# Performance work log

Measured on AMD Instinct MI355X. Metric: run time of the kernel, lower is better.

## Reference

```python
import jax, jax.numpy as jnp
import numpy as np

N = 100000       # nodes
E = 1600000      # edges (avg degree 16)
F_IN = 20        # NUM_FEATURES
H = 128          # hidden_channels
EPS = 1e-5       # GraphNorm eps


def setup_inputs() -> dict:
    key = jax.random.key(0)
    ks = jax.random.split(key, 24)
    s = 0.05
    inp = {
        "x": jax.random.normal(ks[0], (N, F_IN), jnp.float32),
        "edge_index": jax.random.randint(ks[1], (2, E), 0, N, dtype=jnp.int32),
    }
    # SAGEConv params: lin_l (neighbors, with bias), lin_r (root, no bias)
    dims = [(F_IN, H), (H, H), (H, H)]
    k = 2
    for i, (din, dout) in enumerate(dims):
        inp[f"Wl{i}"] = jax.random.normal(ks[k], (dout, din), jnp.float32) * s; k += 1
        inp[f"bl{i}"] = jnp.zeros((dout,), jnp.float32)
        inp[f"Wr{i}"] = jax.random.normal(ks[k], (dout, din), jnp.float32) * s; k += 1
        # GraphNorm: weight, bias, mean_scale (alpha)
        inp[f"gw{i}"] = jnp.ones((dout,), jnp.float32)
        inp[f"gb{i}"] = jnp.zeros((dout,), jnp.float32)
        inp[f"ga{i}"] = jnp.ones((dout,), jnp.float32)
    # MLP head: 128 -> 64 -> 32 -> 1
    inp["hW1"] = jax.random.normal(ks[k], (64, H), jnp.float32) * s; k += 1
    inp["hb1"] = jnp.zeros((64,), jnp.float32)
    inp["hW2"] = jax.random.normal(ks[k], (32, 64), jnp.float32) * s; k += 1
    inp["hb2"] = jnp.zeros((32,), jnp.float32)
    inp["hW3"] = jax.random.normal(ks[k], (1, 32), jnp.float32) * s; k += 1
    inp["hb3"] = jnp.zeros((1,), jnp.float32)
    return inp


def _sage(x, src, dst, Wl, bl, Wr):
    # mean aggregation of source features at destination nodes
    deg = jax.ops.segment_sum(jnp.ones((src.shape[0],), x.dtype), dst, num_segments=N)
    agg = jax.ops.segment_sum(x[src], dst, num_segments=N)
    agg = agg / jnp.maximum(deg, 1.0)[:, None]
    return agg @ Wl.T + bl + x @ Wr.T


def _graphnorm(x, w, b, a):
    # single graph (batch=None): stats over all nodes, per channel
    mean = jnp.mean(x, axis=0)
    c = x - a * mean
    var = jnp.mean(c * c, axis=0)
    return w * c * jax.lax.rsqrt(var + EPS) + b


def reference(x, edge_index,
              Wl0, bl0, Wr0, gw0, gb0, ga0,
              Wl1, bl1, Wr1, gw1, gb1, ga1,
              Wl2, bl2, Wr2, gw2, gb2, ga2,
              hW1, hb1, hW2, hb2, hW3, hb3):
    src, dst = edge_index[0], edge_index[1]
    layers = [(Wl0, bl0, Wr0, gw0, gb0, ga0),
              (Wl1, bl1, Wr1, gw1, gb1, ga1),
              (Wl2, bl2, Wr2, gw2, gb2, ga2)]
    h = x
    for (Wl, bl, Wr, gw, gb, ga) in layers:
        h = _sage(h, src, dst, Wl, bl, Wr)
        h = _graphnorm(h, gw, gb, ga)
        h = jax.nn.gelu(h, approximate=False)  # dropout: eval mode (identity)
    h = jax.nn.gelu(h @ hW1.T + hb1, approximate=False)
    h = jax.nn.gelu(h @ hW2.T + hb2, approximate=False)
    out = jax.nn.sigmoid(h @ hW3.T + hb3)
    return out.squeeze(-1)  # [N]
```

## Files before the change

kernel.cpp:

```cpp
#include <hip/hip_runtime.h>
#include <hip/hip_bf16.h>
#include <math.h>

#define NN 100000
#define EE 1600000
#define FIN 20
#define HH 128
#define NBUK 391
#define FILLB 196
#define MMB 782

typedef __attribute__((ext_vector_type(8))) short bf16x8;
typedef __attribute__((ext_vector_type(4))) float f32x4;

__device__ __forceinline__ unsigned short f2b(float x) {
    unsigned int b = __float_as_uint(x);
    unsigned int r = b + 0x7fffu + ((b >> 16) & 1u);
    return (unsigned short)(r >> 16);
}
__device__ __forceinline__ float lof(unsigned int u) { return __uint_as_float(u << 16); }
__device__ __forceinline__ float hif(unsigned int u) { return __uint_as_float(u & 0xffff0000u); }

__device__ __forceinline__ float gelu_exact(float z) {
    return 0.5f * z * (1.0f + erff(z * 0.70710678118654752f));
}

__global__ __launch_bounds__(256) void kb_cnt(const int* __restrict__ dst,
                                              int* __restrict__ bcnt) {
    __shared__ int c[NBUK];
    int t = threadIdx.x;
    for (int i = t; i < NBUK; i += 256) c[i] = 0;
    __syncthreads();
    int e0 = blockIdx.x * 8192;
    #pragma unroll 4
    for (int i = 0; i < 32; ++i) {
        int e = e0 + i * 256 + t;
        if (e < EE) atomicAdd(&c[dst[e] >> 8], 1);
    }
    __syncthreads();
    for (int i = t; i < NBUK; i += 256) if (c[i]) atomicAdd(&bcnt[i], c[i]);
}

__global__ void kb_scan(const int* __restrict__ bcnt, int* __restrict__ bbase,
                        int* __restrict__ cursor) {
    __shared__ int sh[512];
    int t = threadIdx.x;
    int v = (t < NBUK) ? bcnt[t] : 0;
    sh[t] = v;
    __syncthreads();
    for (int off = 1; off < 512; off <<= 1) {
        int add = (t >= off) ? sh[t - off] : 0;
        __syncthreads();
        sh[t] += add;
        __syncthreads();
    }
    if (t < NBUK) {
        int ex = sh[t] - v;
        bbase[t] = ex;
        cursor[t] = ex;
    }
    if (t == NBUK - 1) bbase[NBUK] = sh[t];
}

__global__ __launch_bounds__(256) void kb_fill(const int* __restrict__ src,
        const int* __restrict__ dst, int* __restrict__ cursor,
        unsigned int* __restrict__ pairs) {
    __shared__ int cnt[NBUK], base[NBUK], boff[NBUK];
    int t = threadIdx.x;
    for (int i = t; i < NBUK; i += 256) { cnt[i] = 0; boff[i] = 0; }
    __syncthreads();
    int e0 = blockIdx.x * 8192;
    #pragma unroll 4
    for (int i = 0; i < 32; ++i) {
        int e = e0 + i * 256 + t;
        if (e < EE) atomicAdd(&cnt[dst[e] >> 8], 1);
    }
    __syncthreads();
    for (int i = t; i < NBUK; i += 256)
        if (cnt[i]) base[i] = atomicAdd(&cursor[i], cnt[i]);
    __syncthreads();
    #pragma unroll 4
    for (int i = 0; i < 32; ++i) {
        int e = e0 + i * 256 + t;
        if (e < EE) {
            int d = dst[e];
            int b = d >> 8;
            int pos = base[b] + atomicAdd(&boff[b], 1);
            pairs[pos] = (unsigned int)src[e] | ((unsigned int)(d & 255) << 17);
        }
    }
}

__global__ __launch_bounds__(256) void kb_csr(const unsigned int* __restrict__ pairs,
        const int* __restrict__ bbase, int* __restrict__ row_start,
        int* __restrict__ deg, float* __restrict__ invdeg, int* __restrict__ col) {
    __shared__ int ldeg[256];
    __shared__ int lcnt[256];
    int b = blockIdx.x, t = threadIdx.x;
    int e0 = bbase[b], e1 = bbase[b + 1];
    ldeg[t] = 0;
    lcnt[t] = 0;
    __syncthreads();
    for (int e = e0 + t; e < e1; e += 256) atomicAdd(&ldeg[pairs[e] >> 17], 1);
    __syncthreads();
    int d = ldeg[t];
    for (int off = 1; off < 256; off <<= 1) {
        int add = (t >= off) ? ldeg[t - off] : 0;
        __syncthreads();
        ldeg[t] += add;
        __syncthreads();
    }
    int n = b * 256 + t;
    if (n < NN) {
        row_start[n] = e0 + ldeg[t] - d;
        deg[n] = d;
        invdeg[n] = 1.0f / fmaxf((float)d, 1.0f);
    }
    __syncthreads();
    for (int e = e0 + t; e < e1; e += 256) {
        unsigned int p = pairs[e];
        int dL = p >> 17;
        int pos = e0 + (dL ? ldeg[dL - 1] : 0) + atomicAdd(&lcnt[dL], 1);
        col[pos] = (int)(p & 0x1FFFFu);
    }
}

__global__ __launch_bounds__(256) void k_packxb(const float* __restrict__ x,
        unsigned short* __restrict__ xb) {
    int id = blockIdx.x * 256 + threadIdx.x;
    if (id >= NN * 32) return;
    int n = id >> 5, k = id & 31;
    xb[id] = f2b((k < FIN) ? x[n * FIN + k] : 0.0f);
}

__global__ __launch_bounds__(256) void k_packx(const float* __restrict__ x,
        unsigned short* __restrict__ A0) {
    int id = blockIdx.x * 256 + threadIdx.x;
    int n = id >> 6, k = id & 63;
    if (n >= NN) return;
    if (k < FIN) return;
    float v = (k >= 32 && k < 32 + FIN) ? x[n * FIN + (k - 32)] : 0.0f;
    A0[id] = f2b(v);
}

__global__ __launch_bounds__(256) void k_agg0(const unsigned int* __restrict__ xb32,
        const int* __restrict__ rs, const int* __restrict__ deg,
        const float* __restrict__ inv, const int* __restrict__ col,
        unsigned short* __restrict__ A0) {
    int g = threadIdx.x >> 4;
    int l = threadIdx.x & 15;
    int n = blockIdx.x * 16 + g;
    if (n >= NN) return;
    int s = rs[n], d = deg[n];
    float a0 = 0.0f, a1 = 0.0f;
    int j = 0;
    for (; j + 1 < d; j += 2) {
        int c0 = col[s + j], c1 = col[s + j + 1];
        unsigned int u0 = xb32[c0 * 16 + l];
        unsigned int u1 = xb32[c1 * 16 + l];
        a0 += lof(u0) + lof(u1);
        a1 += hif(u0) + hif(u1);
    }
    if (j < d) {
        unsigned int u = xb32[col[s + j] * 16 + l];
        a0 += lof(u);
        a1 += hif(u);
    }
    if (l < 10) {
        float iv = inv[n];
        unsigned int o = (unsigned int)f2b(a0 * iv) | ((unsigned int)f2b(a1 * iv) << 16);
        ((unsigned int*)A0)[(size_t)n * 32 + l] = o;
    }
}

__global__ void k_pack0(const float* __restrict__ Wl, const float* __restrict__ Wr,
                        unsigned short* __restrict__ Wt) {
    int id = blockIdx.x * 256 + threadIdx.x;
    int c = id >> 6, k = id & 63;
    float v = 0.0f;
    if (k < FIN) v = Wl[c * FIN + k];
    else if (k >= 32 && k < 32 + FIN) v = Wr[c * FIN + (k - 32)];
    Wt[id] = f2b(v);
}

__global__ __launch_bounds__(64) void k_aggb(const unsigned short* __restrict__ hB,
        const int* __restrict__ rs, const int* __restrict__ deg,
        const float* __restrict__ inv, const int* __restrict__ col,
        unsigned short* __restrict__ aggB) {
    int n = blockIdx.x;
    int t = threadIdx.x;
    int s = rs[n], d = deg[n];
    const unsigned int* h32 = (const unsigned int*)hB;
    float a0 = 0.0f, a1 = 0.0f;
    int j = 0;
    for (; j + 3 < d; j += 4) {
        int c0 = col[s + j], c1 = col[s + j + 1];
        int c2 = col[s + j + 2], c3 = col[s + j + 3];
        unsigned int u0 = h32[(size_t)c0 * 64 + t];
        unsigned int u1 = h32[(size_t)c1 * 64 + t];
        unsigned int u2 = h32[(size_t)c2 * 64 + t];
        unsigned int u3 = h32[(size_t)c3 * 64 + t];
        a0 += lof(u0) + lof(u1) + lof(u2) + lof(u3);
        a1 += hif(u0) + hif(u1) + hif(u2) + hif(u3);
    }
    for (; j < d; ++j) {
        unsigned int u = h32[(size_t)col[s + j] * 64 + t];
        a0 += lof(u);
        a1 += hif(u);
    }
    float iv = inv[n];
    unsigned int o = (unsigned int)f2b(a0 * iv) | ((unsigned int)f2b(a1 * iv) << 16);
    ((unsigned int*)aggB)[(size_t)n * 64 + t] = o;
}

__global__ void k_pack_main(const float* __restrict__ Wl, const float* __restrict__ Wr,
                            unsigned short* __restrict__ Wt) {
    int id = blockIdx.x * 256 + threadIdx.x;
    int c = id >> 8, k = id & 255;
    float v = (k < HH) ? Wl[c * HH + k] : Wr[c * HH + (k - HH)];
    Wt[id] = f2b(v);
}

__global__ void k_pack_head(const float* __restrict__ hW1, const float* __restrict__ hW2,
                            const float* __restrict__ hb1, const float* __restrict__ hb2,
                            unsigned short* __restrict__ W1b, unsigned short* __restrict__ W2b,
                            float* __restrict__ bH1, float* __restrict__ bH2) {
    int id = blockIdx.x * 256 + threadIdx.x;
    if (id < 8192) {
        W1b[id] = f2b(hW1[id]);
    } else if (id < 8192 + 2048) {
        W2b[id - 8192] = f2b(hW2[id - 8192]);
    } else if (id < 8192 + 2048 + 64) {
        bH1[id - 8192 - 2048] = hb1[id - 8192 - 2048];
    } else if (id < 8192 + 2048 + 96) {
        bH2[id - 8192 - 2048 - 64] = hb2[id - 8192 - 2048 - 64];
    }
}

__global__ __launch_bounds__(256) void k_mm(const unsigned short* __restrict__ A0,
        const unsigned short* __restrict__ A1, int c0, int kChunks, int lda,
        const unsigned short* __restrict__ B, int ldb,
        const float* __restrict__ bias, unsigned short* __restrict__ outB,
        float* __restrict__ psPart, float* __restrict__ pqPart, int M) {
    __shared__ __align__(16) unsigned short As[128 * 40];
    __shared__ __align__(16) unsigned short Bs[128 * 40];
    __shared__ float redS[2][128], redQ[2][128];
    const int tid = threadIdx.x;
    const int m0 = blockIdx.x * 128;
    const int w = tid >> 6, lane = tid & 63;
    const int wr = w >> 1, wc = w & 1;
    const int m16 = lane & 15, q = lane >> 4;

    f32x4 acc[4][4];
    #pragma unroll
    for (int i = 0; i < 4; ++i)
        #pragma unroll
        for (int j = 0; j < 4; ++j) acc[i][j] = (f32x4){0.f, 0.f, 0.f, 0.f};

    for (int chunk = 0; chunk < kChunks; ++chunk) {
        const unsigned short* A = (chunk < c0) ? A0 : A1;
        const int kb = (chunk - ((chunk < c0) ? 0 : c0)) * 32;
        #pragma unroll
        for (int it = 0; it < 2; ++it) {
            int s = tid + it * 256;
            int r = s >> 2, p = s & 3;
            int gm = m0 + r;
            uint4 v = make_uint4(0u, 0u, 0u, 0u);
            if (gm < M) v = *(const uint4*)(A + (size_t)gm * lda + kb + p * 8);
            *(uint4*)&As[r * 40 + p * 8] = v;
        }
        {
            const int kbB = chunk * 32;
            #pragma unroll
            for (int it = 0; it < 2; ++it) {
                int s = tid + it * 256;
                int r = s >> 2, p = s & 3;
                uint4 v = *(const uint4*)(B + (size_t)r * ldb + kbB + p * 8);
                *(uint4*)&Bs[r * 40 + p * 8] = v;
            }
        }
        __syncthreads();
        bf16x8 af[4], bfr[4];
        #pragma unroll
        for (int i = 0; i < 4; ++i)
            af[i] = *(const bf16x8*)&As[(wr * 64 + i * 16 + m16) * 40 + q * 8];
        #pragma unroll
        for (int j = 0; j < 4; ++j)
            bfr[j] = *(const bf16x8*)&Bs[(wc * 64 + j * 16 + m16) * 40 + q * 8];
        #pragma unroll
        for (int i = 0; i < 4; ++i)
            #pragma unroll
            for (int j = 0; j < 4; ++j)
                acc[i][j] = __builtin_amdgcn_mfma_f32_16x16x32_bf16(af[i], bfr[j], acc[i][j], 0, 0, 0);
        __syncthreads();
    }

    float cs[4] = {0.f, 0.f, 0.f, 0.f};
    float cq[4] = {0.f, 0.f, 0.f, 0.f};
    #pragma unroll
    for (int i = 0; i < 4; ++i) {
        int mBase = m0 + wr * 64 + i * 16 + q * 4;
        #pragma unroll
        for (int j = 0; j < 4; ++j) {
            int cc = wc * 64 + j * 16 + m16;
            float bv = bias[cc];
            #pragma unroll
            for (int r = 0; r < 4; ++r) {
                int m = mBase + r;
                float v = (m < M) ? (acc[i][j][r] + bv) : 0.0f;
                if (m < M) outB[(size_t)m * 128 + cc] = f2b(v);
                cs[j] += v;
                cq[j] += v * v;
            }
        }
    }
    #pragma unroll
    for (int msk = 16; msk < 64; msk <<= 1) {
        #pragma unroll
        for (int j = 0; j < 4; ++j) {
            cs[j] += __shfl_xor(cs[j], msk, 64);
            cq[j] += __shfl_xor(cq[j], msk, 64);
        }
    }
    if (q == 0) {
        #pragma unroll
        for (int j = 0; j < 4; ++j) {
            int cc = wc * 64 + j * 16 + m16;
            redS[wr][cc] = cs[j];
            redQ[wr][cc] = cq[j];
        }
    }
    __syncthreads();
    if (tid < 128) {
        psPart[(size_t)blockIdx.x * 128 + tid] = redS[0][tid] + redS[1][tid];
        pqPart[(size_t)blockIdx.x * 128 + tid] = redQ[0][tid] + redQ[1][tid];
    }
}

__global__ __launch_bounds__(1024) void k_gn_final(const float* __restrict__ ps,
        const float* __restrict__ pq, const float* __restrict__ gw,
        const float* __restrict__ gb, const float* __restrict__ ga,
        float* __restrict__ cA, float* __restrict__ cB, int nP) {
    __shared__ float shs[8][128], shq[8][128];
    int c = threadIdx.x & 127, sl = threadIdx.x >> 7;
    float s = 0.0f, q = 0.0f;
    for (int b = sl; b < nP; b += 8) {
        s += ps[b * 128 + c];
        q += pq[b * 128 + c];
    }
    shs[sl][c] = s;
    shq[sl][c] = q;
    __syncthreads();
    if (threadIdx.x < 128) {
        float S = 0.0f, Q = 0.0f;
        #pragma unroll
        for (int i = 0; i < 8; ++i) { S += shs[i][c]; Q += shq[i][c]; }
        float mean = S / (float)NN;
        float msq  = Q / (float)NN;
        float a = ga[c];
        float var = msq - mean * mean * a * (2.0f - a);
        float rstd = rsqrtf(var + 1e-5f);
        float A = gw[c] * rstd;
        cA[c] = A;
        cB[c] = gb[c] - a * mean * A;
    }
}

__global__ __launch_bounds__(256) void k_gn_apply(const unsigned short* __restrict__ yB,
        const float* __restrict__ cA, const float* __restrict__ cB,
        unsigned short* __restrict__ hB) {
    int i = blockIdx.x * 256 + threadIdx.x;
    if (i >= NN * 16) return;
    int g = i & 15;
    uint4 v = ((const uint4*)yB)[i];
    float4 A0 = ((const float4*)cA)[g * 2];
    float4 A1 = ((const float4*)cA)[g * 2 + 1];
    float4 B0 = ((const float4*)cB)[g * 2];
    float4 B1 = ((const float4*)cB)[g * 2 + 1];
    unsigned int o0 = (unsigned int)f2b(gelu_exact(lof(v.x) * A0.x + B0.x))
                    | ((unsigned int)f2b(gelu_exact(hif(v.x) * A0.y + B0.y)) << 16);
    unsigned int o1 = (unsigned int)f2b(gelu_exact(lof(v.y) * A0.z + B0.z))
                    | ((unsigned int)f2b(gelu_exact(hif(v.y) * A0.w + B0.w)) << 16);
    unsigned int o2 = (unsigned int)f2b(gelu_exact(lof(v.z) * A1.x + B1.x))
                    | ((unsigned int)f2b(gelu_exact(hif(v.z) * A1.y + B1.y)) << 16);
    unsigned int o3 = (unsigned int)f2b(gelu_exact(lof(v.w) * A1.z + B1.z))
                    | ((unsigned int)f2b(gelu_exact(hif(v.w) * A1.w + B1.w)) << 16);
    ((uint4*)hB)[i] = make_uint4(o0, o1, o2, o3);
}

__global__ __launch_bounds__(256) void k_headf(const unsigned short* __restrict__ hB,
        const unsigned short* __restrict__ W1b, const float* __restrict__ b1,
        const unsigned short* __restrict__ W2b, const float* __restrict__ b2,
        const float* __restrict__ W3, const float* __restrict__ b3,
        float* __restrict__ out) {
    __shared__ __align__(16) char pool[23040];
    unsigned short* As  = (unsigned short*)pool;
    unsigned short* Bs  = (unsigned short*)(pool + 10240);
    unsigned short* As2 = (unsigned short*)pool;
    unsigned short* Bs2 = (unsigned short*)(pool + 18432);
    const int tid = threadIdx.x;
    const int m0 = blockIdx.x * 128;
    const int w = tid >> 6, lane = tid & 63;
    const int m16 = lane & 15, q = lane >> 4;

    #pragma unroll
    for (int it = 0; it < 8; ++it) {
        int i = tid + it * 256;
        if (i < 2048) Bs2[(i >> 6) * 72 + (i & 63)] = W2b[i];
    }

    f32x4 acc1[2][4];
    #pragma unroll
    for (int i = 0; i < 2; ++i)
        #pragma unroll
        for (int j = 0; j < 4; ++j) acc1[i][j] = (f32x4){0.f, 0.f, 0.f, 0.f};

    for (int chunk = 0; chunk < 4; ++chunk) {
        const int kb = chunk * 32;
        #pragma unroll
        for (int it = 0; it < 2; ++it) {
            int s = tid + it * 256;
            int r = s >> 2, p = s & 3;
            int gm = m0 + r;
            uint4 v = make_uint4(0u, 0u, 0u, 0u);
            if (gm < NN) v = *(const uint4*)(hB + (size_t)gm * 128 + kb + p * 8);
            *(uint4*)&As[r * 40 + p * 8] = v;
        }
        {
            int r = tid >> 2, p = tid & 3;
            uint4 v = *(const uint4*)(W1b + (size_t)r * 128 + kb + p * 8);
            *(uint4*)&Bs[r * 40 + p * 8] = v;
        }
        __syncthreads();
        bf16x8 af[2], bfr[4];
        #pragma unroll
        for (int i = 0; i < 2; ++i)
            af[i] = *(const bf16x8*)&As[(w * 32 + i * 16 + m16) * 40 + q * 8];
        #pragma unroll
        for (int j = 0; j < 4; ++j)
            bfr[j] = *(const bf16x8*)&Bs[(j * 16 + m16) * 40 + q * 8];
        #pragma unroll
        for (int i = 0; i < 2; ++i)
            #pragma unroll
            for (int j = 0; j < 4; ++j)
                acc1[i][j] = __builtin_amdgcn_mfma_f32_16x16x32_bf16(af[i], bfr[j], acc1[i][j], 0, 0, 0);
        __syncthreads();
    }

    {
        float b1v[4];
        #pragma unroll
        for (int j = 0; j < 4; ++j) b1v[j] = b1[j * 16 + m16];
        #pragma unroll
        for (int i = 0; i < 2; ++i) {
            int mloc = w * 32 + i * 16 + q * 4;
            #pragma unroll
            for (int j = 0; j < 4; ++j) {
                int c = j * 16 + m16;
                #pragma unroll
                for (int r = 0; r < 4; ++r)
                    As2[(mloc + r) * 72 + c] = f2b(gelu_exact(acc1[i][j][r] + b1v[j]));
            }
        }
    }
    __syncthreads();

    f32x4 acc2[2][2];
    #pragma unroll
    for (int i = 0; i < 2; ++i)
        #pragma unroll
        for (int j = 0; j < 2; ++j) acc2[i][j] = (f32x4){0.f, 0.f, 0.f, 0.f};
    #pragma unroll
    for (int kc = 0; kc < 2; ++kc) {
        bf16x8 a2[2], bf2[2];
        #pragma unroll
        for (int i = 0; i < 2; ++i)
            a2[i] = *(const bf16x8*)&As2[(w * 32 + i * 16 + m16) * 72 + kc * 32 + q * 8];
        #pragma unroll
        for (int j = 0; j < 2; ++j)
            bf2[j] = *(const bf16x8*)&Bs2[(j * 16 + m16) * 72 + kc * 32 + q * 8];
        #pragma unroll
        for (int i = 0; i < 2; ++i)
            #pragma unroll
            for (int j = 0; j < 2; ++j)
                acc2[i][j] = __builtin_amdgcn_mfma_f32_16x16x32_bf16(a2[i], bf2[j], acc2[i][j], 0, 0, 0);
    }

    float w3a = W3[m16], w3b = W3[16 + m16];
    float b2a = b2[m16], b2b = b2[16 + m16];
    float p[8];
    #pragma unroll
    for (int i = 0; i < 2; ++i)
        #pragma unroll
        for (int r = 0; r < 4; ++r) {
            float za = gelu_exact(acc2[i][0][r] + b2a);
            float zb = gelu_exact(acc2[i][1][r] + b2b);
            p[i * 4 + r] = za * w3a + zb * w3b;
        }
    #pragma unroll
    for (int msk = 1; msk < 16; msk <<= 1)
        #pragma unroll
        for (int k = 0; k < 8; ++k) p[k] += __shfl_xor(p[k], msk, 64);
    if (m16 == 0) {
        float b3v = b3[0];
        #pragma unroll
        for (int i = 0; i < 2; ++i)
            #pragma unroll
            for (int r = 0; r < 4; ++r) {
                int m = m0 + w * 32 + i * 16 + q * 4 + r;
                if (m < NN) out[m] = 1.0f / (1.0f + expf(-(p[i * 4 + r] + b3v)));
            }
    }
}

extern "C" void kernel_launch(void* const* d_in, const int* in_sizes, int n_in,
                              void* d_out, int out_size, void* d_ws, size_t ws_size,
                              hipStream_t stream) {
    const float* x   = (const float*)d_in[0];
    const int*   ei  = (const int*)d_in[1];
    const float* Wl0 = (const float*)d_in[2];
    const float* bl0 = (const float*)d_in[3];
    const float* Wr0 = (const float*)d_in[4];
    const float* gw0 = (const float*)d_in[5];
    const float* gb0 = (const float*)d_in[6];
    const float* ga0 = (const float*)d_in[7];
    const float* Wl1 = (const float*)d_in[8];
    const float* bl1 = (const float*)d_in[9];
    const float* Wr1 = (const float*)d_in[10];
    const float* gw1 = (const float*)d_in[11];
    const float* gb1 = (const float*)d_in[12];
    const float* ga1 = (const float*)d_in[13];
    const float* Wl2 = (const float*)d_in[14];
    const float* bl2 = (const float*)d_in[15];
    const float* Wr2 = (const float*)d_in[16];
    const float* gw2 = (const float*)d_in[17];
    const float* gb2 = (const float*)d_in[18];
    const float* ga2 = (const float*)d_in[19];
    const float* hW1 = (const float*)d_in[20];
    const float* hb1 = (const float*)d_in[21];
    const float* hW2 = (const float*)d_in[22];
    const float* hb2 = (const float*)d_in[23];
    const float* hW3 = (const float*)d_in[24];
    const float* hb3 = (const float*)d_in[25];
    float* out = (float*)d_out;

    size_t off = 0;
    auto carve = [&](size_t bytes) -> void* {
        void* p = (void*)((char*)d_ws + off);
        off += (bytes + 255) & ~(size_t)255;
        return p;
    };
    int*   bcnt      = (int*)carve((size_t)NBUK * 4);
    int*   bbase     = (int*)carve((size_t)(NBUK + 1) * 4);
    int*   cursor    = (int*)carve((size_t)NBUK * 4);
    unsigned int* pairs = (unsigned int*)carve((size_t)EE * 4);
    int*   deg       = (int*)carve((size_t)NN * 4);
    int*   row_start = (int*)carve((size_t)NN * 4);
    float* invdeg    = (float*)carve((size_t)NN * 4);
    int*   colarr    = (int*)carve((size_t)EE * 4);
    unsigned short* xb    = (unsigned short*)carve((size_t)NN * 32 * 2);
    unsigned short* Wt0   = (unsigned short*)carve(128 * 64 * 2);
    unsigned short* Wt2   = (unsigned short*)carve(128 * 256 * 2);
    unsigned short* W1b   = (unsigned short*)carve(64 * 128 * 2);
    unsigned short* W2b   = (unsigned short*)carve(32 * 64 * 2);
    float* biasH1    = (float*)carve(64 * 4);
    float* biasH2    = (float*)carve(32 * 4);
    float* ps        = (float*)carve((size_t)MMB * 128 * 4);
    float* pq        = (float*)carve((size_t)MMB * 128 * 4);
    float* coefA     = (float*)carve(128 * 4);
    float* coefB     = (float*)carve(128 * 4);
    unsigned short* A0pack = (unsigned short*)carve((size_t)NN * 64 * 2);
    unsigned short* hB   = (unsigned short*)carve((size_t)NN * HH * 2);
    unsigned short* aggB = (unsigned short*)carve((size_t)NN * HH * 2);
    unsigned short* yB   = (unsigned short*)carve((size_t)NN * HH * 2);
    if (off > ws_size) return;

    const int* src = ei;
    const int* dst = ei + EE;

    hipMemsetAsync(bcnt, 0, (size_t)NBUK * 4, stream);
    kb_cnt<<<FILLB, 256, 0, stream>>>(dst, bcnt);
    kb_scan<<<1, 512, 0, stream>>>(bcnt, bbase, cursor);
    kb_fill<<<FILLB, 256, 0, stream>>>(src, dst, cursor, pairs);
    kb_csr<<<NBUK, 256, 0, stream>>>(pairs, bbase, row_start, deg, invdeg, colarr);

    k_packxb<<<(NN * 32 + 255) / 256, 256, 0, stream>>>(x, xb);
    k_packx<<<(NN * 64 + 255) / 256, 256, 0, stream>>>(x, A0pack);
    k_agg0<<<(NN + 15) / 16, 256, 0, stream>>>((const unsigned int*)xb, row_start,
                                               deg, invdeg, colarr, A0pack);
    k_pack0<<<32, 256, 0, stream>>>(Wl0, Wr0, Wt0);
    k_mm<<<MMB, 256, 0, stream>>>(A0pack, A0pack, 2, 2, 64, Wt0, 64, bl0, yB, ps, pq, NN);
    k_gn_final<<<1, 1024, 0, stream>>>(ps, pq, gw0, gb0, ga0, coefA, coefB, MMB);
    k_gn_apply<<<(NN * 16 + 255) / 256, 256, 0, stream>>>(yB, coefA, coefB, hB);

    const float* WlL[2] = {Wl1, Wl2};
    const float* blL[2] = {bl1, bl2};
    const float* WrL[2] = {Wr1, Wr2};
    const float* gwL[2] = {gw1, gw2};
    const float* gbL[2] = {gb1, gb2};
    const float* gaL[2] = {ga1, ga2};
    for (int l = 0; l < 2; ++l) {
        k_pack_main<<<128, 256, 0, stream>>>(WlL[l], WrL[l], Wt2);
        k_aggb<<<NN, 64, 0, stream>>>(hB, row_start, deg, invdeg, colarr, aggB);
        k_mm<<<MMB, 256, 0, stream>>>(aggB, hB, 4, 8, 128, Wt2, 256, blL[l],
                                      yB, ps, pq, NN);
        k_gn_final<<<1, 1024, 0, stream>>>(ps, pq, gwL[l], gbL[l], gaL[l], coefA, coefB, MMB);
        k_gn_apply<<<(NN * 16 + 255) / 256, 256, 0, stream>>>(yB, coefA, coefB, hB);
    }

    k_pack_head<<<(8192 + 2048 + 96 + 255) / 256, 256, 0, stream>>>(
        hW1, hW2, hb1, hb2, W1b, W2b, biasH1, biasH2);
    k_headf<<<MMB, 256, 0, stream>>>(hB, W1b, biasH1, W2b, biasH2, hW3, hb3, out);
}
```

Baseline: 562.9 us.

## Merge pack kernels into one launch and widen gather loads in aggregation

All the separate packing kernels (x to bf16, A0 pad, layer-0/1/2 weights, head weights) become one fused launch issued before CSR construction, which removes several small launches. The layer-1/2 aggregation now handles one node per wavefront, with four edge rows in flight and 16-byte loads per lane, finishing with a shuffle reduction. Layer-0 aggregation uses the same scheme with 8-byte loads. The intent is more memory-level parallelism in the neighbour gathers and less launch overhead. The cost is extra cross-lane shuffles, and lanes sit idle on low-degree nodes.

```diff
diff --git a/kernel.cpp b/kernel.cpp
--- a/kernel.cpp
+++ b/kernel.cpp
@@ -20,6 +20,9 @@
 }
 __device__ __forceinline__ float lof(unsigned int u) { return __uint_as_float(u << 16); }
 __device__ __forceinline__ float hif(unsigned int u) { return __uint_as_float(u & 0xffff0000u); }
+__device__ __forceinline__ unsigned int pk2(float a, float b) {
+    return (unsigned int)f2b(a) | ((unsigned int)f2b(b) << 16);
+}
 
 __device__ __forceinline__ float gelu_exact(float z) {
     return 0.5f * z * (1.0f + erff(z * 0.70710678118654752f));
@@ -125,115 +128,151 @@
     }
 }
 
-__global__ __launch_bounds__(256) void k_packxb(const float* __restrict__ x,
-        unsigned short* __restrict__ xb) {
+#define XB_N  (NN * 32)
+#define A0_N  (NN * 64)
+#define PACK_TOTAL (XB_N + A0_N + 8192 + 32768 + 32768 + 8192 + 2048 + 64 + 32)
+__global__ __launch_bounds__(256) void k_pack_all(const float* __restrict__ x,
+        const float* __restrict__ Wl0, const float* __restrict__ Wr0,
+        const float* __restrict__ Wl1, const float* __restrict__ Wr1,
+        const float* __restrict__ Wl2, const float* __restrict__ Wr2,
+        const float* __restrict__ hW1, const float* __restrict__ hW2,
+        const float* __restrict__ hb1, const float* __restrict__ hb2,
+        unsigned short* __restrict__ xb, unsigned short* __restrict__ A0,
+        unsigned short* __restrict__ Wt0, unsigned short* __restrict__ Wt2a,
+        unsigned short* __restrict__ Wt2b, unsigned short* __restrict__ W1b,
+        unsigned short* __restrict__ W2b, float* __restrict__ bH1,
+        float* __restrict__ bH2) {
     int id = blockIdx.x * 256 + threadIdx.x;
-    if (id >= NN * 32) return;
-    int n = id >> 5, k = id & 31;
-    xb[id] = f2b((k < FIN) ? x[n * FIN + k] : 0.0f);
-}
-
-__global__ __launch_bounds__(256) void k_packx(const float* __restrict__ x,
-        unsigned short* __restrict__ A0) {
-    int id = blockIdx.x * 256 + threadIdx.x;
-    int n = id >> 6, k = id & 63;
-    if (n >= NN) return;
-    if (k < FIN) return;
-    float v = (k >= 32 && k < 32 + FIN) ? x[n * FIN + (k - 32)] : 0.0f;
-    A0[id] = f2b(v);
-}
-
-__global__ __launch_bounds__(256) void k_agg0(const unsigned int* __restrict__ xb32,
+    if (id < XB_N) {
+        int n = id >> 5, k = id & 31;
+        xb[id] = f2b((k < FIN) ? x[n * FIN + k] : 0.0f);
+        return;
+    }
+    id -= XB_N;
+    if (id < A0_N) {
+        int k = id & 63;
+        if (k >= FIN) {
+            int n = id >> 6;
+            float v = (k >= 32 && k < 32 + FIN) ? x[n * FIN + (k - 32)] : 0.0f;
+            A0[id] = f2b(v);
+        }
+        return;
+    }
+    id -= A0_N;
+    if (id < 8192) {
+        int c = id >> 6, k = id & 63;
+        float v = 0.0f;
+        if (k < FIN) v = Wl0[c * FIN + k];
+        else if (k >= 32 && k < 32 + FIN) v = Wr0[c * FIN + (k - 32)];
+        Wt0[id] = f2b(v);
+        return;
+    }
+    id -= 8192;
+    if (id < 32768) {
+        int c = id >> 8, k = id & 255;
+        Wt2a[id] = f2b((k < HH) ? Wl1[c * HH + k] : Wr1[c * HH + (k - HH)]);
+        return;
+    }
+    id -= 32768;
+    if (id < 32768) {
+        int c = id >> 8, k = id & 255;
+        Wt2b[id] = f2b((k < HH) ? Wl2[c * HH + k] : Wr2[c * HH + (k - HH)]);
+        return;
+    }
+    id -= 32768;
+    if (id < 8192) { W1b[id] = f2b(hW1[id]); return; }
+    id -= 8192;
+    if (id < 2048) { W2b[id] = f2b(hW2[id]); return; }
+    id -= 2048;
+    if (id < 64) { bH1[id] = hb1[id]; return; }
+    id -= 64;
+    if (id < 32) { bH2[id] = hb2[id]; return; }
+}
+
+__global__ __launch_bounds__(256) void k_agg0(const uint2* __restrict__ xb2,
         const int* __restrict__ rs, const int* __restrict__ deg,
         const float* __restrict__ inv, const int* __restrict__ col,
         unsigned short* __restrict__ A0) {
-    int g = threadIdx.x >> 4;
-    int l = threadIdx.x & 15;
-    int n = blockIdx.x * 16 + g;
+    int wid = threadIdx.x >> 6;
+    int lane = threadIdx.x & 63;
+    int er = lane >> 3;
+    int c8 = lane & 7;
+    int n = blockIdx.x * 4 + wid;
     if (n >= NN) return;
     int s = rs[n], d = deg[n];
-    float a0 = 0.0f, a1 = 0.0f;
-    int j = 0;
-    for (; j + 1 < d; j += 2) {
-        int c0 = col[s + j], c1 = col[s + j + 1];
-        unsigned int u0 = xb32[c0 * 16 + l];
-        unsigned int u1 = xb32[c1 * 16 + l];
-        a0 += lof(u0) + lof(u1);
-        a1 += hif(u0) + hif(u1);
-    }
-    if (j < d) {
-        unsigned int u = xb32[col[s + j] * 16 + l];
-        a0 += lof(u);
-        a1 += hif(u);
-    }
-    if (l < 10) {
+    float a0 = 0.f, a1 = 0.f, a2 = 0.f, a3 = 0.f;
+    for (int j0 = 0; j0 < d; j0 += 8) {
+        int j = j0 + er;
+        if (j < d) {
+            int c = col[s + j];
+            uint2 v = xb2[(size_t)c * 8 + c8];
+            a0 += lof(v.x); a1 += hif(v.x);
+            a2 += lof(v.y); a3 += hif(v.y);
+        }
+    }
+    #pragma unroll
+    for (int m = 8; m < 64; m <<= 1) {
+        a0 += __shfl_xor(a0, m, 64);
+        a1 += __shfl_xor(a1, m, 64);
+        a2 += __shfl_xor(a2, m, 64);
+        a3 += __shfl_xor(a3, m, 64);
+    }
+    if (er == 0 && c8 < 5) {
         float iv = inv[n];
-        unsigned int o = (unsigned int)f2b(a0 * iv) | ((unsigned int)f2b(a1 * iv) << 16);
-        ((unsigned int*)A0)[(size_t)n * 32 + l] = o;
-    }
-}
-
-__global__ void k_pack0(const float* __restrict__ Wl, const float* __restrict__ Wr,
-                        unsigned short* __restrict__ Wt) {
-    int id = blockIdx.x * 256 + threadIdx.x;
-    int c = id >> 6, k = id & 63;
-    float v = 0.0f;
-    if (k < FIN) v = Wl[c * FIN + k];
-    else if (k >= 32 && k < 32 + FIN) v = Wr[c * FIN + (k - 32)];
-    Wt[id] = f2b(v);
-}
-
-__global__ __launch_bounds__(64) void k_aggb(const unsigned short* __restrict__ hB,
+        uint2 o;
+        o.x = pk2(a0 * iv, a1 * iv);
+        o.y = pk2(a2 * iv, a3 * iv);
+        ((uint2*)A0)[(size_t)n * 16 + c8] = o;
+    }
+}
+
+__global__ __launch_bounds__(256) void k_aggb(const unsigned short* __restrict__ hB,
         const int* __restrict__ rs, const int* __restrict__ deg,
         const float* __restrict__ inv, const int* __restrict__ col,
         unsigned short* __restrict__ aggB) {
-    int n = blockIdx.x;
-    int t = threadIdx.x;
+    int wid = threadIdx.x >> 6;
+    int lane = threadIdx.x & 63;
+    int er = lane >> 4;
+    int c16 = lane & 15;
+    int n = blockIdx.x * 4 + wid;
+    if (n >= NN) return;
     int s = rs[n], d = deg[n];
-    const unsigned int* h32 = (const unsigned int*)hB;
-    float a0 = 0.0f, a1 = 0.0f;
-    int j = 0;
-    for (; j + 3 < d; j += 4) {
-        int c0 = col[s + j], c1 = col[s + j + 1];
-        int c2 = col[s + j + 2], c3 = col[s + j + 3];
-        unsigned int u0 = h32[(size_t)c0 * 64 + t];
-        unsigned int u1 = h32[(size_t)c1 * 64 + t];
-        unsigned int u2 = h32[(size_t)c2 * 64 + t];
-        unsigned int u3 = h32[(size_t)c3 * 64 + t];
-        a0 += lof(u0) + lof(u1) + lof(u2) + lof(u3);
-        a1 += hif(u0) + hif(u1) + hif(u2) + hif(u3);
-    }
-    for (; j < d; ++j) {
-        unsigned int u = h32[(size_t)col[s + j] * 64 + t];
-        a0 += lof(u);
-        a1 += hif(u);
-    }
-    float iv = inv[n];
-    unsigned int o = (unsigned int)f2b(a0 * iv) | ((unsigned int)f2b(a1 * iv) << 16);
-    ((unsigned int*)aggB)[(size_t)n * 64 + t] = o;
-}
-
-__global__ void k_pack_main(const float* __restrict__ Wl, const float* __restrict__ Wr,
-                            unsigned short* __restrict__ Wt) {
-    int id = blockIdx.x * 256 + threadIdx.x;
-    int c = id >> 8, k = id & 255;
-    float v = (k < HH) ? Wl[c * HH + k] : Wr[c * HH + (k - HH)];
-    Wt[id] = f2b(v);
-}
-
-__global__ void k_pack_head(const float* __restrict__ hW1, const float* __restrict__ hW2,
-                            const float* __restrict__ hb1, const float* __restrict__ hb2,
-                            unsigned short* __restrict__ W1b, unsigned short* __restrict__ W2b,
-                            float* __restrict__ bH1, float* __restrict__ bH2) {
-    int id = blockIdx.x * 256 + threadIdx.x;
-    if (id < 8192) {
-        W1b[id] = f2b(hW1[id]);
-    } else if (id < 8192 + 2048) {
-        W2b[id - 8192] = f2b(hW2[id - 8192]);
-    } else if (id < 8192 + 2048 + 64) {
-        bH1[id - 8192 - 2048] = hb1[id - 8192 - 2048];
-    } else if (id < 8192 + 2048 + 96) {
-        bH2[id - 8192 - 2048 - 64] = hb2[id - 8192 - 2048 - 64];
+    const uint4* h4 = (const uint4*)hB;
+    float a0 = 0.f, a1 = 0.f, a2 = 0.f, a3 = 0.f;
+    float a4 = 0.f, a5 = 0.f, a6 = 0.f, a7 = 0.f;
+    for (int j0 = 0; j0 < d; j0 += 8) {
+        #pragma unroll
+        for (int u = 0; u < 2; ++u) {
+            int j = j0 + u * 4 + er;
+            if (j < d) {
+                int c = col[s + j];
+                uint4 v = h4[(size_t)c * 16 + c16];
+                a0 += lof(v.x); a1 += hif(v.x);
+                a2 += lof(v.y); a3 += hif(v.y);
+                a4 += lof(v.z); a5 += hif(v.z);
+                a6 += lof(v.w); a7 += hif(v.w);
+            }
+        }
+    }
+    #pragma unroll
+    for (int m = 16; m < 64; m <<= 1) {
+        a0 += __shfl_xor(a0, m, 64);
+        a1 += __shfl_xor(a1, m, 64);
+        a2 += __shfl_xor(a2, m, 64);
+        a3 += __shfl_xor(a3, m, 64);
+        a4 += __shfl_xor(a4, m, 64);
+        a5 += __shfl_xor(a5, m, 64);
+        a6 += __shfl_xor(a6, m, 64);
+        a7 += __shfl_xor(a7, m, 64);
+    }
+    if (er == 0) {
+        float iv = inv[n];
+        uint4 o;
+        o.x = pk2(a0 * iv, a1 * iv);
+        o.y = pk2(a2 * iv, a3 * iv);
+        o.z = pk2(a4 * iv, a5 * iv);
+        o.w = pk2(a6 * iv, a7 * iv);
+        ((uint4*)aggB)[(size_t)n * 16 + c16] = o;
     }
 }
 
@@ -377,14 +416,14 @@
     float4 A1 = ((const float4*)cA)[g * 2 + 1];
     float4 B0 = ((const float4*)cB)[g * 2];
     float4 B1 = ((const float4*)cB)[g * 2 + 1];
-    unsigned int o0 = (unsigned int)f2b(gelu_exact(lof(v.x) * A0.x + B0.x))
-                    | ((unsigned int)f2b(gelu_exact(hif(v.x) * A0.y + B0.y)) << 16);
-    unsigned int o1 = (unsigned int)f2b(gelu_exact(lof(v.y) * A0.z + B0.z))
-                    | ((unsigned int)f2b(gelu_exact(hif(v.y) * A0.w + B0.w)) << 16);
-    unsigned int o2 = (unsigned int)f2b(gelu_exact(lof(v.z) * A1.x + B1.x))
-                    | ((unsigned int)f2b(gelu_exact(hif(v.z) * A1.y + B1.y)) << 16);
-    unsigned int o3 = (unsigned int)f2b(gelu_exact(lof(v.w) * A1.z + B1.z))
-                    | ((unsigned int)f2b(gelu_exact(hif(v.w) * A1.w + B1.w)) << 16);
+    unsigned int o0 = pk2(gelu_exact(lof(v.x) * A0.x + B0.x),
+                          gelu_exact(hif(v.x) * A0.y + B0.y));
+    unsigned int o1 = pk2(gelu_exact(lof(v.y) * A0.z + B0.z),
+                          gelu_exact(hif(v.y) * A0.w + B0.w));
+    unsigned int o2 = pk2(gelu_exact(lof(v.z) * A1.x + B1.x),
+                          gelu_exact(hif(v.z) * A1.y + B1.y));
+    unsigned int o3 = pk2(gelu_exact(lof(v.w) * A1.z + B1.z),
+                          gelu_exact(hif(v.w) * A1.w + B1.w));
     ((uint4*)hB)[i] = make_uint4(o0, o1, o2, o3);
 }
 
@@ -560,7 +599,8 @@
     int*   colarr    = (int*)carve((size_t)EE * 4);
     unsigned short* xb    = (unsigned short*)carve((size_t)NN * 32 * 2);
     unsigned short* Wt0   = (unsigned short*)carve(128 * 64 * 2);
-    unsigned short* Wt2   = (unsigned short*)carve(128 * 256 * 2);
+    unsigned short* Wt2a  = (unsigned short*)carve(128 * 256 * 2);
+    unsigned short* Wt2b  = (unsigned short*)carve(128 * 256 * 2);
     unsigned short* W1b   = (unsigned short*)carve(64 * 128 * 2);
     unsigned short* W2b   = (unsigned short*)carve(32 * 64 * 2);
     float* biasH1    = (float*)carve(64 * 4);
@@ -579,36 +619,32 @@
     const int* dst = ei + EE;
 
     hipMemsetAsync(bcnt, 0, (size_t)NBUK * 4, stream);
+    k_pack_all<<<(PACK_TOTAL + 255) / 256, 256, 0, stream>>>(
+        x, Wl0, Wr0, Wl1, Wr1, Wl2, Wr2, hW1, hW2, hb1, hb2,
+        xb, A0pack, Wt0, Wt2a, Wt2b, W1b, W2b, biasH1, biasH2);
     kb_cnt<<<FILLB, 256, 0, stream>>>(dst, bcnt);
     kb_scan<<<1, 512, 0, stream>>>(bcnt, bbase, cursor);
     kb_fill<<<FILLB, 256, 0, stream>>>(src, dst, cursor, pairs);
     kb_csr<<<NBUK, 256, 0, stream>>>(pairs, bbase, row_start, deg, invdeg, colarr);
 
-    k_packxb<<<(NN * 32 + 255) / 256, 256, 0, stream>>>(x, xb);
-    k_packx<<<(NN * 64 + 255) / 256, 256, 0, stream>>>(x, A0pack);
-    k_agg0<<<(NN + 15) / 16, 256, 0, stream>>>((const unsigned int*)xb, row_start,
-                                               deg, invdeg, colarr, A0pack);
-    k_pack0<<<32, 256, 0, stream>>>(Wl0, Wr0, Wt0);
+    k_agg0<<<(NN + 3) / 4, 256, 0, stream>>>((const uint2*)xb, row_start,
+                                             deg, invdeg, colarr, A0pack);
     k_mm<<<MMB, 256, 0, stream>>>(A0pack, A0pack, 2, 2, 64, Wt0, 64, bl0, yB, ps, pq, NN);
     k_gn_final<<<1, 1024, 0, stream>>>(ps, pq, gw0, gb0, ga0, coefA, coefB, MMB);
     k_gn_apply<<<(NN * 16 + 255) / 256, 256, 0, stream>>>(yB, coefA, coefB, hB);
 
-    const float* WlL[2] = {Wl1, Wl2};
+    const unsigned short* WtL[2] = {Wt2a, Wt2b};
     const float* blL[2] = {bl1, bl2};
-    const float* WrL[2] = {Wr1, Wr2};
     const float* gwL[2] = {gw1, gw2};
     const float* gbL[2] = {gb1, gb2};
     const float* gaL[2] = {ga1, ga2};
     for (int l = 0; l < 2; ++l) {
-        k_pack_main<<<128, 256, 0, stream>>>(WlL[l], WrL[l], Wt2);
-        k_aggb<<<NN, 64, 0, stream>>>(hB, row_start, deg, invdeg, colarr, aggB);
-        k_mm<<<MMB, 256, 0, stream>>>(aggB, hB, 4, 8, 128, Wt2, 256, blL[l],
+        k_aggb<<<(NN + 3) / 4, 256, 0, stream>>>(hB, row_start, deg, invdeg, colarr, aggB);
+        k_mm<<<MMB, 256, 0, stream>>>(aggB, hB, 4, 8, 128, WtL[l], 256, blL[l],
                                       yB, ps, pq, NN);
         k_gn_final<<<1, 1024, 0, stream>>>(ps, pq, gwL[l], gbL[l], gaL[l], coefA, coefB, MMB);
         k_gn_apply<<<(NN * 16 + 255) / 256, 256, 0, stream>>>(yB, coefA, coefB, hB);
     }
 
-    k_pack_head<<<(8192 + 2048 + 96 + 255) / 256, 256, 0, stream>>>(
-        hW1, hW2, hb1, hb2, W1b, W2b, biasH1, biasH2);
     k_headf<<<MMB, 256, 0, stream>>>(hB, W1b, biasH1, W2b, biasH2, hW3, hb3, out);
 }
```

New measurement: 587.7 us. +4.4%, slower.
